# Optimization experiments

Hardware: AMD Instinct MI355X
Metric: run time of the kernel (lower is better)

## Reference

```python
import jax, jax.numpy as jnp
import numpy as np

HALF_STEP = 0.05
NUM_V = 10  # clamp(floor(0.5/0.05), 2, 1000)
EPS = 1e-6


def _normalize(x):
    return x / (jnp.linalg.norm(x, axis=-1, keepdims=True) + EPS)


def _ragged_structure(edge_points_np):
    # Concrete (numpy) ragged-grid index structure: per-edge horizontal sample
    # counts from edge length, exclusive-cumsum offsets, repeat_interleave ids.
    sp = edge_points_np[:, 0]
    cd = edge_points_np[:, 1] - sp
    cl = np.linalg.norm(cd + EPS, axis=1)
    num_h = np.clip((cl // HALF_STEP).astype(np.int64), 2, 1000)  # [N]
    total_x = int(num_h.sum())
    begin = np.concatenate([[0], np.cumsum(num_h)[:-1]])           # roll-based exclusive cumsum
    eid_x = np.repeat(np.arange(len(num_h)), num_h)                # [total_x] edge id per x-sample
    pos_x = np.arange(total_x) - begin[eid_x]                      # dx integer position within edge
    eid = np.repeat(eid_x, NUM_V)                                  # [P] edge id per sample point
    pos_x_full = np.repeat(pos_x, NUM_V).astype(np.float32)        # coords_x integer part
    dy_idx = np.tile(np.arange(NUM_V), total_x).astype(np.float32) # coords_y integer part
    denom_full = np.repeat((num_h - 1)[eid_x], NUM_V).astype(np.float32)
    return (jnp.asarray(eid), jnp.asarray(pos_x_full), jnp.asarray(denom_full),
            jnp.asarray(dy_idx))


def _sample_img(img, uv):
    # img [1,3,H,W]; uv [P,2] in [0,1) -> bilinear sample (align_corners style)
    im = img[0]
    H, W = im.shape[1], im.shape[2]
    x = uv[:, 0] * (W - 1)
    y = uv[:, 1] * (H - 1)
    x0 = jnp.floor(x).astype(jnp.int32)
    y0 = jnp.floor(y).astype(jnp.int32)
    x1 = jnp.clip(x0 + 1, 0, W - 1)
    y1 = jnp.clip(y0 + 1, 0, H - 1)
    wx = (x - x0)[None]
    wy = (y - y0)[None]
    g = lambda yy, xx: im[:, yy, xx]  # [3,P] gather
    out = (g(y0, x0) * (1 - wx) * (1 - wy) + g(y0, x1) * wx * (1 - wy)
           + g(y1, x0) * (1 - wx) * wy + g(y1, x1) * wx * wy)
    return out.T  # [P,3]


def _forward(edge_points, intrinsic1, intrinsic2, extrinsic1, extrinsic2,
             rgb1, rgb2, eid, pos_x, denom, dy_idx):
    start = edge_points[:, 0]
    cur_dir = edge_points[:, 1] - start
    next_dir = edge_points[:, 3] - edge_points[:, 1]
    prev_dir = edge_points[:, 0] - edge_points[:, 2]
    cur_len = jnp.linalg.norm(cur_dir + EPS, axis=1)
    cur_dir = cur_dir / cur_len[:, None]
    cur_normal = _normalize(jnp.cross(cur_dir, next_dir))
    flip = cur_normal[:, 2] > 0  # dot with (0,0,1) > 0 -> flip sign
    cur_normal = jnp.where(flip[:, None], -cur_normal, cur_normal)
    cur_up = _normalize(jnp.cross(cur_normal, cur_dir))
    prev_normal = _normalize(jnp.cross(prev_dir, cur_dir))

    # ragged per-edge sample grid (repeat_interleave realized via gather on eid)
    coords_x = pos_x / denom * cur_len[eid]          # [P]
    coords_y = dy_idx / (NUM_V - 1) * 0.5            # [P]
    pts = (cur_dir[eid] * coords_x[:, None]
           + cur_up[eid] * coords_y[:, None]
           + start[eid])                              # [P,3]

    # view 1 projection + bilinear sample
    uv1 = pts @ intrinsic1.T
    uv1 = jnp.clip(uv1[:, :2] / uv1[:, 2:3], 0.0, 0.999999)
    s1 = _sample_img(rgb1, uv1)

    # view 2: K2_homog @ E2 @ inv(E1) applied to homogeneous points
    K2h = jnp.eye(4, dtype=pts.dtype).at[:3, :3].set(intrinsic2)
    T = K2h @ extrinsic2 @ jnp.linalg.inv(extrinsic1)
    ph = jnp.concatenate([pts, jnp.ones_like(pts[:, :1])], axis=1)
    uv2 = ph @ T.T
    uv2 = jnp.clip(uv2[:, :2] / uv2[:, 2:3], 0.0, 0.999999)
    s2 = _sample_img(rgb2, uv2)

    similarity_loss = jnp.mean((s1 - s2) ** 2)
    normal_loss = jnp.mean(1.0 - jnp.sum(cur_normal * prev_normal, axis=1)) / 2.0
    obs_normal = _normalize(jnp.cross(edge_points[:, 0], edge_points[:, 1]))
    snp = jnp.minimum(jnp.abs(jnp.sum(cur_up * obs_normal, axis=1)), 0.5)
    normalization_loss = jnp.mean(1.0 - snp / 0.5)
    return jnp.stack([similarity_loss, normal_loss, normalization_loss])


def setup_inputs() -> dict:
    key = jax.random.key(0)
    k0, k1, k2 = jax.random.split(key, 3)
    N, H, W = 10000, 1500, 2000
    # camera-space edge endpoints/neighbors, pushed in front of the camera
    edge_points = jax.random.normal(k0, (N, 4, 3), dtype=jnp.float32) \
        + jnp.array([0.0, 0.0, 6.0], dtype=jnp.float32)
    intrinsic1 = jnp.array([[0.3, 0.0, 0.5], [0.0, 0.3, 0.5], [0.0, 0.0, 1.0]],
                           dtype=jnp.float32)
    intrinsic2 = intrinsic1
    extrinsic1 = jnp.eye(4, dtype=jnp.float32)
    extrinsic2 = jnp.eye(4, dtype=jnp.float32).at[:3, 3].set(
        jnp.array([0.1, 0.0, 0.0], dtype=jnp.float32))
    rgb1 = jax.random.uniform(k1, (1, 3, H, W), dtype=jnp.float32)
    rgb2 = jax.random.uniform(k2, (1, 3, H, W), dtype=jnp.float32)
    return {"edge_points": edge_points, "intrinsic1": intrinsic1,
            "intrinsic2": intrinsic2, "extrinsic1": extrinsic1,
            "extrinsic2": extrinsic2, "rgb1": rgb1, "rgb2": rgb2}


def reference(edge_points, intrinsic1, intrinsic2, extrinsic1, extrinsic2,
              rgb1, rgb2):
    eid, pos_x, denom, dy_idx = _ragged_structure(np.asarray(edge_points))
    return _forward(edge_points, intrinsic1, intrinsic2, extrinsic1,
                    extrinsic2, rgb1, rgb2, eid, pos_x, denom, dy_idx)
```

## Files before the change

kernel.cpp:

```cpp
#include <hip/hip_runtime.h>
#include <math.h>

#define EPSF 1e-6f
#define NUM_V 10
#define W_IMG 2000
#define H_IMG 1500
#define HW_IMG (W_IMG * H_IMG)
#define TH_QUAD (H_IMG - 1)
#define SAMPLE_BLOCKS 2048
#define NPART (SAMPLE_BLOCKS * 4)
#define MAX_CHUNKS 80

struct Ctrl {
    int cursor;
    int pad0, pad1, pad2;
    double accNL;
    double accZL;
    double accC;
};

__device__ __forceinline__ void cross3(const float a[3], const float b[3], float c[3]) {
    c[0] = a[1] * b[2] - a[2] * b[1];
    c[1] = a[2] * b[0] - a[0] * b[2];
    c[2] = a[0] * b[1] - a[1] * b[0];
}
__device__ __forceinline__ float dot3(const float a[3], const float b[3]) {
    return a[0] * b[0] + a[1] * b[1] + a[2] * b[2];
}
__device__ __forceinline__ float norm3(const float a[3]) {
    return sqrtf(a[0] * a[0] + a[1] * a[1] + a[2] * a[2]);
}

__device__ void make_T(const float* __restrict__ K2, const float* __restrict__ E1,
                       const float* __restrict__ E2, float* __restrict__ T) {
    float M[4][8];
    for (int i = 0; i < 4; ++i)
        for (int j = 0; j < 4; ++j) {
            M[i][j] = E1[i * 4 + j];
            M[i][j + 4] = (i == j) ? 1.f : 0.f;
        }
    for (int col = 0; col < 4; ++col) {
        int piv = col;
        float best = fabsf(M[col][col]);
        for (int r = col + 1; r < 4; ++r) {
            float v = fabsf(M[r][col]);
            if (v > best) { best = v; piv = r; }
        }
        if (piv != col)
            for (int j = 0; j < 8; ++j) {
                float t = M[col][j]; M[col][j] = M[piv][j]; M[piv][j] = t;
            }
        float d = 1.f / M[col][col];
        for (int j = 0; j < 8; ++j) M[col][j] *= d;
        for (int r = 0; r < 4; ++r) {
            if (r == col) continue;
            float f = M[r][col];
            for (int j = 0; j < 8; ++j) M[r][j] -= f * M[col][j];
        }
    }
    float E[4][4];
    for (int i = 0; i < 4; ++i)
        for (int j = 0; j < 4; ++j) {
            float s = 0.f;
            for (int k = 0; k < 4; ++k) s += E2[i * 4 + k] * M[k][j + 4];
            E[i][j] = s;
        }
    for (int i = 0; i < 4; ++i)
        for (int j = 0; j < 4; ++j) {
            float s;
            if (i < 3) {
                s = 0.f;
                for (int k = 0; k < 3; ++k) s += K2[i * 3 + k] * E[k][j];
            } else {
                s = E[3][j];
            }
            T[i * 4 + j] = s;
        }
}

__device__ __forceinline__ unsigned quant565(float r, float g, float b) {
    unsigned r5 = (unsigned)fmaf(r, 31.f, 0.5f);
    unsigned g6 = (unsigned)fmaf(g, 63.f, 0.5f);
    unsigned b5 = (unsigned)fmaf(b, 31.f, 0.5f);
    return (r5 << 11) | (g6 << 5) | b5;
}

__global__ __launch_bounds__(256) void prep_kernel(
    const float* __restrict__ ep, int N, int GB, int RPB,
    const float* __restrict__ K2v, const float* __restrict__ E1, const float* __restrict__ E2,
    const float* __restrict__ rgb1, const float* __restrict__ rgb2,
    float* __restrict__ T, Ctrl* __restrict__ ctrl,
    float4* __restrict__ geo, unsigned* __restrict__ sched,
    uint2* __restrict__ t1, uint2* __restrict__ t2) {
    const int b = blockIdx.x;
    if (b < RPB) {
        const int gpi = TH_QUAD * (W_IMG / 4);
        const int t = b * 256 + threadIdx.x;
        if (t >= 2 * gpi) return;
        const int img = t >= gpi;
        const int g = t - img * gpi;
        const int y = g / (W_IMG / 4);
        const int x = (g - y * (W_IMG / 4)) * 4;
        const float* src = img ? rgb2 : rgb1;
        uint2* dst = img ? t2 : t1;
        unsigned pk[2][5];
#pragma unroll
        for (int r = 0; r < 2; ++r) {
            const int yy = y + r;
            float px[3][5];
#pragma unroll
            for (int c = 0; c < 3; ++c) {
                const float* bp = src + (size_t)c * HW_IMG + (size_t)yy * W_IMG + x;
                float4 a = *(const float4*)bp;
                float e = (x + 4 < W_IMG) ? bp[4] : a.w;
                px[c][0] = a.x; px[c][1] = a.y; px[c][2] = a.z; px[c][3] = a.w; px[c][4] = e;
            }
#pragma unroll
            for (int k = 0; k < 5; ++k) pk[r][k] = quant565(px[0][k], px[1][k], px[2][k]);
        }
        uint2* o = dst + (size_t)y * W_IMG + x;
        uint4 s0 = make_uint4(pk[0][0] | (pk[0][1] << 16), pk[1][0] | (pk[1][1] << 16),
                              pk[0][1] | (pk[0][2] << 16), pk[1][1] | (pk[1][2] << 16));
        uint4 s1 = make_uint4(pk[0][2] | (pk[0][3] << 16), pk[1][2] | (pk[1][3] << 16),
                              pk[0][3] | (pk[0][4] << 16), pk[1][3] | (pk[1][4] << 16));
        *(uint4*)(o + 0) = s0;
        *(uint4*)(o + 2) = s1;
        return;
    }
    if (b < RPB + GB) {
        const int e = (b - RPB) * 256 + threadIdx.x;
        float nl = 0.f, zl = 0.f;
        int cn = 0;
        if (e < N) {
            const float4* P4 = (const float4*)(ep + (size_t)e * 12);
            float4 a4 = P4[0], b4 = P4[1], c4 = P4[2];
            float p0[3] = {a4.x, a4.y, a4.z};
            float p1[3] = {a4.w, b4.x, b4.y};
            float p2[3] = {b4.z, b4.w, c4.x};
            float p3[3] = {c4.y, c4.z, c4.w};
            float cd[3] = {p1[0] - p0[0], p1[1] - p0[1], p1[2] - p0[2]};
            float nd[3] = {p3[0] - p1[0], p3[1] - p1[1], p3[2] - p1[2]};
            float pd[3] = {p0[0] - p2[0], p0[1] - p2[1], p0[2] - p2[2]};
            float ce[3] = {cd[0] + EPSF, cd[1] + EPSF, cd[2] + EPSF};
            float clen = norm3(ce);
            float dir[3] = {cd[0] / clen, cd[1] / clen, cd[2] / clen};
            float cnv[3];
            cross3(dir, nd, cnv);
            float n1 = norm3(cnv) + EPSF;
            cnv[0] /= n1; cnv[1] /= n1; cnv[2] /= n1;
            if (cnv[2] > 0.f) { cnv[0] = -cnv[0]; cnv[1] = -cnv[1]; cnv[2] = -cnv[2]; }
            float up[3];
            cross3(cnv, dir, up);
            float n2 = norm3(up) + EPSF;
            up[0] /= n2; up[1] /= n2; up[2] /= n2;
            float pn[3];
            cross3(pd, dir, pn);
            float n3 = norm3(pn) + EPSF;
            pn[0] /= n3; pn[1] /= n3; pn[2] /= n3;
            float obs[3];
            cross3(p0, p1, obs);
            float n4 = norm3(obs) + EPSF;
            obs[0] /= n4; obs[1] /= n4; obs[2] /= n4;
            int nh = (int)floorf(clen / 0.05f);
            nh = max(2, min(1000, nh));
            nl = 1.f - dot3(cnv, pn);
            float snp = fminf(fabsf(dot3(up, obs)), 0.5f);
            zl = 1.f - snp * 2.f;
            const int nsamp = nh * NUM_V;
            cn = nsamp;
            geo[3 * e + 0] = make_float4(p0[0], p0[1], p0[2], clen);
            geo[3 * e + 1] = make_float4(dir[0], dir[1], dir[2], (float)(nh - 1));
            geo[3 * e + 2] = make_float4(up[0], up[1], up[2], __int_as_float(nsamp));
            const int nc = (nsamp + 127) / 128;
            const int basee = atomicAdd(&ctrl->cursor, nc);
            const unsigned tag = ((unsigned)e) << 8;
            for (int j = 0; j < nc; ++j) sched[basee + j] = tag | (unsigned)j;
        }
#pragma unroll
        for (int off = 32; off > 0; off >>= 1) {
            nl += __shfl_down(nl, off);
            zl += __shfl_down(zl, off);
            cn += __shfl_down(cn, off);
        }
        if ((threadIdx.x & 63) == 0) {
            atomicAdd(&ctrl->accNL, (double)nl);
            atomicAdd(&ctrl->accZL, (double)zl);
            atomicAdd(&ctrl->accC, (double)cn);
        }
        return;
    }
    if (threadIdx.x == 0) make_T(K2v, E1, E2, T);
}

__device__ __forceinline__ float mse565(uint2 qa, uint2 qb, float wxa, float wya, float wxb,
                                        float wyb) {
    float wa00 = (1.f - wxa) * (1.f - wya), wa01 = wxa * (1.f - wya);
    float wa10 = (1.f - wxa) * wya, wa11 = wxa * wya;
    float wb00 = (1.f - wxb) * (1.f - wyb), wb01 = wxb * (1.f - wyb);
    float wb10 = (1.f - wxb) * wyb, wb11 = wxb * wyb;
    unsigned a00 = qa.x & 0xffffu, a01 = qa.x >> 16, a10 = qa.y & 0xffffu, a11 = qa.y >> 16;
    unsigned b00 = qb.x & 0xffffu, b01 = qb.x >> 16, b10 = qb.y & 0xffffu, b11 = qb.y >> 16;
    float ra = fmaf((float)(a00 >> 11), wa00, fmaf((float)(a01 >> 11), wa01,
               fmaf((float)(a10 >> 11), wa10, (float)(a11 >> 11) * wa11)));
    float rb = fmaf((float)(b00 >> 11), wb00, fmaf((float)(b01 >> 11), wb01,
               fmaf((float)(b10 >> 11), wb10, (float)(b11 >> 11) * wb11)));
    float ga = fmaf((float)((a00 >> 5) & 63u), wa00, fmaf((float)((a01 >> 5) & 63u), wa01,
               fmaf((float)((a10 >> 5) & 63u), wa10, (float)((a11 >> 5) & 63u) * wa11)));
    float gb = fmaf((float)((b00 >> 5) & 63u), wb00, fmaf((float)((b01 >> 5) & 63u), wb01,
               fmaf((float)((b10 >> 5) & 63u), wb10, (float)((b11 >> 5) & 63u) * wb11)));
    float ba = fmaf((float)(a00 & 31u), wa00, fmaf((float)(a01 & 31u), wa01,
               fmaf((float)(a10 & 31u), wa10, (float)(a11 & 31u) * wa11)));
    float bb = fmaf((float)(b00 & 31u), wb00, fmaf((float)(b01 & 31u), wb01,
               fmaf((float)(b10 & 31u), wb10, (float)(b11 & 31u) * wb11)));
    float dr = (ra - rb) * (1.f / 31.f);
    float dg = (ga - gb) * (1.f / 63.f);
    float db = (ba - bb) * (1.f / 31.f);
    return fmaf(dr, dr, fmaf(dg, dg, db * db));
}

__global__ __launch_bounds__(256) void sample_kernel(
    const float4* __restrict__ geo, const float* __restrict__ K1, const float* __restrict__ T,
    const uint2* __restrict__ im1, const uint2* __restrict__ im2,
    const unsigned* __restrict__ sched, const int* __restrict__ total_p,
    double* __restrict__ part) {
    const int wid = blockIdx.x * 4 + (threadIdx.x >> 6);
    const int lane = threadIdx.x & 63;
    const int nw = gridDim.x * 4;
    const int total = *total_p;

    const float k00 = K1[0], k01 = K1[1], k02 = K1[2];
    const float k10 = K1[3], k11 = K1[4], k12 = K1[5];
    const float k20 = K1[6], k21 = K1[7], k22 = K1[8];
    const float t00 = T[0], t01 = T[1], t02 = T[2], t03 = T[3];
    const float t10 = T[4], t11 = T[5], t12 = T[6], t13 = T[7];
    const float t20 = T[8], t21 = T[9], t22 = T[10], t23 = T[11];

    float lsum = 0.f;
    for (int base = wid; base < total; base += 2 * nw) {
        const int idxB = base + nw;
        const bool has2 = idxB < total;
        const unsigned sA = (unsigned)__builtin_amdgcn_readfirstlane((int)sched[base]);
        const unsigned sB =
            has2 ? (unsigned)__builtin_amdgcn_readfirstlane((int)sched[idxB]) : sA;
        const int eA = (int)(sA >> 8), kA = (int)(sA & 255u);
        const int eB = (int)(sB >> 8), kB = (int)(sB & 255u);
        const float4 a0 = geo[3 * eA + 0], a1 = geo[3 * eA + 1], a2 = geo[3 * eA + 2];
        const float4 b0 = geo[3 * eB + 0], b1 = geo[3 * eB + 1], b2 = geo[3 * eB + 2];
        const int nsA = __float_as_int(a2.w), nsB = __float_as_int(b2.w);
        const float lodA = a0.w * __builtin_amdgcn_rcpf(a1.w);
        const float lodB = b0.w * __builtin_amdgcn_rcpf(b1.w);

        int off1[4], off2[4];
        float wx1[4], wy1[4], wx2[4], wy2[4];
        bool ok[4];
#pragma unroll
        for (int j = 0; j < 4; ++j) {
            const int d = j >> 1, h = j & 1;
            const float4 g0 = d ? b0 : a0;
            const float4 g1 = d ? b1 : a1;
            const float4 g2 = d ? b2 : a2;
            const int ns = d ? nsB : nsA;
            const int kk = d ? kB : kA;
            const float lod = d ? lodB : lodA;
            const int i = kk * 128 + h * 64 + lane;
            ok[j] = (i < ns) && (d == 0 || has2);
            const int ic = min(i, ns - 1);
            int px = ic / NUM_V;
            int dy = ic - px * NUM_V;
            float cx = (float)px * lod;
            float cy = (float)dy * (0.5f / 9.0f);
            float X = fmaf(g1.x, cx, fmaf(g2.x, cy, g0.x));
            float Y = fmaf(g1.y, cx, fmaf(g2.y, cy, g0.y));
            float Z = fmaf(g1.z, cx, fmaf(g2.z, cy, g0.z));
            float iw1 = __builtin_amdgcn_rcpf(fmaf(k20, X, fmaf(k21, Y, k22 * Z)));
            float u1 = fminf(fmaxf(fmaf(k00, X, fmaf(k01, Y, k02 * Z)) * iw1, 0.f), 0.999999f);
            float v1 = fminf(fmaxf(fmaf(k10, X, fmaf(k11, Y, k12 * Z)) * iw1, 0.f), 0.999999f);
            float iw2 = __builtin_amdgcn_rcpf(fmaf(t20, X, fmaf(t21, Y, fmaf(t22, Z, t23))));
            float u2 = fminf(
                fmaxf(fmaf(t00, X, fmaf(t01, Y, fmaf(t02, Z, t03))) * iw2, 0.f), 0.999999f);
            float v2 = fminf(
                fmaxf(fmaf(t10, X, fmaf(t11, Y, fmaf(t12, Z, t13))) * iw2, 0.f), 0.999999f);
            float xa = u1 * (float)(W_IMG - 1), ya = v1 * (float)(H_IMG - 1);
            float xb = u2 * (float)(W_IMG - 1), yb = v2 * (float)(H_IMG - 1);
            float fxa = floorf(xa), fya = floorf(ya), fxb = floorf(xb), fyb = floorf(yb);
            off1[j] = (int)fya * W_IMG + (int)fxa;
            off2[j] = (int)fyb * W_IMG + (int)fxb;
            wx1[j] = xa - fxa; wy1[j] = ya - fya;
            wx2[j] = xb - fxb; wy2[j] = yb - fyb;
        }
        uint2 q1[4], q2[4];
#pragma unroll
        for (int j = 0; j < 4; ++j) q1[j] = im1[off1[j]];
#pragma unroll
        for (int j = 0; j < 4; ++j) q2[j] = im2[off2[j]];
#pragma unroll
        for (int j = 0; j < 4; ++j) {
            float v = mse565(q1[j], q2[j], wx1[j], wy1[j], wx2[j], wy2[j]);
            lsum += ok[j] ? v : 0.f;
        }
    }
    double dsum = (double)lsum;
#pragma unroll
    for (int off = 32; off > 0; off >>= 1) dsum += __shfl_down(dsum, off);
    if (lane == 0) part[wid] = dsum;
}

__global__ __launch_bounds__(256) void finalize_kernel(const double* __restrict__ part, int NP,
                                                       const Ctrl* __restrict__ ctrl, int N,
                                                       float* __restrict__ out) {
    __shared__ double s_s[4];
    double s = 0.0;
    for (int i = threadIdx.x; i < NP; i += 256) s += part[i];
#pragma unroll
    for (int off = 32; off > 0; off >>= 1) s += __shfl_down(s, off);
    const int wave = threadIdx.x >> 6;
    if ((threadIdx.x & 63) == 0) s_s[wave] = s;
    __syncthreads();
    if (threadIdx.x == 0) {
        double S = s_s[0] + s_s[1] + s_s[2] + s_s[3];
        double A = ctrl->accNL;
        double B = ctrl->accZL;
        double C = ctrl->accC;
        out[0] = (float)(S / (C * 3.0));
        out[1] = (float)(A / (double)N * 0.5);
        out[2] = (float)(B / (double)N);
    }
}

extern "C" void kernel_launch(void* const* d_in, const int* in_sizes, int n_in, void* d_out,
                              int out_size, void* d_ws, size_t ws_size, hipStream_t stream) {
    const float* ep = (const float*)d_in[0];
    const float* K1 = (const float*)d_in[1];
    const float* K2 = (const float*)d_in[2];
    const float* E1 = (const float*)d_in[3];
    const float* E2 = (const float*)d_in[4];
    const float* rgb1 = (const float*)d_in[5];
    const float* rgb2 = (const float*)d_in[6];
    float* out = (float*)d_out;
    const int N = in_sizes[0] / 12;

    const int GB = (N + 255) / 256;
    const int gpi = TH_QUAD * (W_IMG / 4);
    const int RPB = (2 * gpi + 255) / 256;

    char* p = (char*)d_ws;
    float* T = (float*)p;               p += 256;
    Ctrl* ctrl = (Ctrl*)p;              p += 256;
    float4* geo = (float4*)p;           p += (size_t)3 * N * sizeof(float4);
    p = (char*)(((size_t)p + 255) & ~(size_t)255);
    double* part = (double*)p;          p += (size_t)NPART * sizeof(double);
    p = (char*)(((size_t)p + 255) & ~(size_t)255);
    unsigned* sched = (unsigned*)p;     p += (size_t)N * MAX_CHUNKS * sizeof(unsigned);
    p = (char*)(((size_t)p + 255) & ~(size_t)255);
    uint2* img1 = (uint2*)p;
    uint2* img2 = img1 + (size_t)TH_QUAD * W_IMG;

    hipMemsetAsync(ctrl, 0, sizeof(Ctrl), stream);
    prep_kernel<<<RPB + GB + 1, 256, 0, stream>>>(ep, N, GB, RPB, K2, E1, E2, rgb1, rgb2, T,
                                                  ctrl, geo, sched, img1, img2);
    sample_kernel<<<SAMPLE_BLOCKS, 256, 0, stream>>>(geo, K1, T, img1, img2, sched,
                                                     &ctrl->cursor, part);
    finalize_kernel<<<1, 256, 0, stream>>>(part, NPART, ctrl, N, out);
}
```

Measured before the change: 191.0 us.

## Shrink quantized image to one 32-bit word per pixel with vertical pair packing

The precomputed RGB565 texture changes from 8 bytes per pixel, which held the full 2x2 bilinear quad, to 4 bytes per pixel holding the vertical pair (row y and row y+1). This halves the prep write traffic and the texture footprint, so it fits better in cache. In exchange, the sampler now issues two 32-bit gathers per image per sample (pixel x and x+1) instead of one 64-bit gather. Both kernels also get a min-blocks-per-CU launch bound of 8, which pushes register use down for occupancy.

```diff
diff --git a/kernel.cpp b/kernel.cpp
--- a/kernel.cpp
+++ b/kernel.cpp
@@ -85,13 +85,13 @@
     return (r5 << 11) | (g6 << 5) | b5;
 }
 
-__global__ __launch_bounds__(256) void prep_kernel(
+__global__ __launch_bounds__(256, 8) void prep_kernel(
     const float* __restrict__ ep, int N, int GB, int RPB,
     const float* __restrict__ K2v, const float* __restrict__ E1, const float* __restrict__ E2,
     const float* __restrict__ rgb1, const float* __restrict__ rgb2,
     float* __restrict__ T, Ctrl* __restrict__ ctrl,
     float4* __restrict__ geo, unsigned* __restrict__ sched,
-    uint2* __restrict__ t1, uint2* __restrict__ t2) {
+    unsigned* __restrict__ t1, unsigned* __restrict__ t2) {
     const int b = blockIdx.x;
     if (b < RPB) {
         const int gpi = TH_QUAD * (W_IMG / 4);
@@ -102,29 +102,25 @@
         const int y = g / (W_IMG / 4);
         const int x = (g - y * (W_IMG / 4)) * 4;
         const float* src = img ? rgb2 : rgb1;
-        uint2* dst = img ? t2 : t1;
-        unsigned pk[2][5];
-#pragma unroll
-        for (int r = 0; r < 2; ++r) {
-            const int yy = y + r;
-            float px[3][5];
-#pragma unroll
-            for (int c = 0; c < 3; ++c) {
-                const float* bp = src + (size_t)c * HW_IMG + (size_t)yy * W_IMG + x;
-                float4 a = *(const float4*)bp;
-                float e = (x + 4 < W_IMG) ? bp[4] : a.w;
-                px[c][0] = a.x; px[c][1] = a.y; px[c][2] = a.z; px[c][3] = a.w; px[c][4] = e;
-            }
-#pragma unroll
-            for (int k = 0; k < 5; ++k) pk[r][k] = quant565(px[0][k], px[1][k], px[2][k]);
-        }
-        uint2* o = dst + (size_t)y * W_IMG + x;
-        uint4 s0 = make_uint4(pk[0][0] | (pk[0][1] << 16), pk[1][0] | (pk[1][1] << 16),
-                              pk[0][1] | (pk[0][2] << 16), pk[1][1] | (pk[1][2] << 16));
-        uint4 s1 = make_uint4(pk[0][2] | (pk[0][3] << 16), pk[1][2] | (pk[1][3] << 16),
-                              pk[0][3] | (pk[0][4] << 16), pk[1][3] | (pk[1][4] << 16));
-        *(uint4*)(o + 0) = s0;
-        *(uint4*)(o + 2) = s1;
+        unsigned* dst = img ? t2 : t1;
+        float4 r0[3], r1[3];
+#pragma unroll
+        for (int c = 0; c < 3; ++c) {
+            const float* bp = src + (size_t)c * HW_IMG + (size_t)y * W_IMG + x;
+            r0[c] = *(const float4*)bp;
+            r1[c] = *(const float4*)(bp + W_IMG);
+        }
+        const float* f0r = (const float*)&r0[0]; const float* f1r = (const float*)&r1[0];
+        const float* f0g = (const float*)&r0[1]; const float* f1g = (const float*)&r1[1];
+        const float* f0b = (const float*)&r0[2]; const float* f1b = (const float*)&r1[2];
+        unsigned w[4];
+#pragma unroll
+        for (int k = 0; k < 4; ++k) {
+            unsigned lo = quant565(f0r[k], f0g[k], f0b[k]);
+            unsigned hi = quant565(f1r[k], f1g[k], f1b[k]);
+            w[k] = lo | (hi << 16);
+        }
+        *(uint4*)(dst + (size_t)y * W_IMG + x) = make_uint4(w[0], w[1], w[2], w[3]);
         return;
     }
     if (b < RPB + GB) {
@@ -192,14 +188,14 @@
     if (threadIdx.x == 0) make_T(K2v, E1, E2, T);
 }
 
-__device__ __forceinline__ float mse565(uint2 qa, uint2 qb, float wxa, float wya, float wxb,
-                                        float wyb) {
+__device__ __forceinline__ float mse565(unsigned qa0, unsigned qa1, unsigned qb0, unsigned qb1,
+                                        float wxa, float wya, float wxb, float wyb) {
     float wa00 = (1.f - wxa) * (1.f - wya), wa01 = wxa * (1.f - wya);
     float wa10 = (1.f - wxa) * wya, wa11 = wxa * wya;
     float wb00 = (1.f - wxb) * (1.f - wyb), wb01 = wxb * (1.f - wyb);
     float wb10 = (1.f - wxb) * wyb, wb11 = wxb * wyb;
-    unsigned a00 = qa.x & 0xffffu, a01 = qa.x >> 16, a10 = qa.y & 0xffffu, a11 = qa.y >> 16;
-    unsigned b00 = qb.x & 0xffffu, b01 = qb.x >> 16, b10 = qb.y & 0xffffu, b11 = qb.y >> 16;
+    unsigned a00 = qa0 & 0xffffu, a10 = qa0 >> 16, a01 = qa1 & 0xffffu, a11 = qa1 >> 16;
+    unsigned b00 = qb0 & 0xffffu, b10 = qb0 >> 16, b01 = qb1 & 0xffffu, b11 = qb1 >> 16;
     float ra = fmaf((float)(a00 >> 11), wa00, fmaf((float)(a01 >> 11), wa01,
                fmaf((float)(a10 >> 11), wa10, (float)(a11 >> 11) * wa11)));
     float rb = fmaf((float)(b00 >> 11), wb00, fmaf((float)(b01 >> 11), wb01,
@@ -218,9 +214,9 @@
     return fmaf(dr, dr, fmaf(dg, dg, db * db));
 }
 
-__global__ __launch_bounds__(256) void sample_kernel(
+__global__ __launch_bounds__(256, 8) void sample_kernel(
     const float4* __restrict__ geo, const float* __restrict__ K1, const float* __restrict__ T,
-    const uint2* __restrict__ im1, const uint2* __restrict__ im2,
+    const unsigned* __restrict__ im1, const unsigned* __restrict__ im2,
     const unsigned* __restrict__ sched, const int* __restrict__ total_p,
     double* __restrict__ part) {
     const int wid = blockIdx.x * 4 + (threadIdx.x >> 6);
@@ -288,14 +284,14 @@
             wx1[j] = xa - fxa; wy1[j] = ya - fya;
             wx2[j] = xb - fxb; wy2[j] = yb - fyb;
         }
-        uint2 q1[4], q2[4];
-#pragma unroll
-        for (int j = 0; j < 4; ++j) q1[j] = im1[off1[j]];
-#pragma unroll
-        for (int j = 0; j < 4; ++j) q2[j] = im2[off2[j]];
-#pragma unroll
-        for (int j = 0; j < 4; ++j) {
-            float v = mse565(q1[j], q2[j], wx1[j], wy1[j], wx2[j], wy2[j]);
+        unsigned q1a[4], q1b[4], q2a[4], q2b[4];
+#pragma unroll
+        for (int j = 0; j < 4; ++j) { q1a[j] = im1[off1[j]]; q1b[j] = im1[off1[j] + 1]; }
+#pragma unroll
+        for (int j = 0; j < 4; ++j) { q2a[j] = im2[off2[j]]; q2b[j] = im2[off2[j] + 1]; }
+#pragma unroll
+        for (int j = 0; j < 4; ++j) {
+            float v = mse565(q1a[j], q1b[j], q2a[j], q2b[j], wx1[j], wy1[j], wx2[j], wy2[j]);
             lsum += ok[j] ? v : 0.f;
         }
     }
@@ -352,8 +348,8 @@
     p = (char*)(((size_t)p + 255) & ~(size_t)255);
     unsigned* sched = (unsigned*)p;     p += (size_t)N * MAX_CHUNKS * sizeof(unsigned);
     p = (char*)(((size_t)p + 255) & ~(size_t)255);
-    uint2* img1 = (uint2*)p;
-    uint2* img2 = img1 + (size_t)TH_QUAD * W_IMG;
+    unsigned* img1 = (unsigned*)p;
+    unsigned* img2 = img1 + (size_t)TH_QUAD * W_IMG;
 
     hipMemsetAsync(ctrl, 0, sizeof(Ctrl), stream);
     prep_kernel<<<RPB + GB + 1, 256, 0, stream>>>(ep, N, GB, RPB, K2, E1, E2, rgb1, rgb2, T,
```

Result: faster. 172.2 us (-9.9%).
